# Optimization experiments

Measured on AMD Instinct MI355X. Metric: run time of the kernel, lower is better.

Reference implementation:

```python
import jax, jax.numpy as jnp
import numpy as np

B, T, H, L, V = 256, 1024, 256, 128, 13  # V = FDIM_JOINT_VOCAB_DECODING


def setup_inputs() -> dict:
    key = jax.random.key(0)
    ks = jax.random.split(key, 16)
    s = lambda *sh: 1.0 / np.sqrt(sh[-1])
    inp = {
        "seq_input": jax.random.normal(ks[0], (B, T, V), jnp.float32),
        "latent_vec": jax.random.normal(ks[1], (B, L), jnp.float32),
        "labels": jax.random.randint(ks[2], (B, T), 0, V, jnp.int32),
        "lengths": jax.random.randint(ks[3], (B,), 1, T, jnp.int32),
        # latent_vec_linear: L -> H
        "W_lat": jax.random.normal(ks[4], (H, L), jnp.float32) * s(H, L),
        "b_lat": jnp.zeros((H,), jnp.float32),
        # LSTMCell (PyTorch gate order i,f,g,o)
        "W_ih": jax.random.normal(ks[5], (4 * H, V), jnp.float32) * s(4 * H, V),
        "W_hh": jax.random.normal(ks[6], (4 * H, H), jnp.float32) * s(4 * H, H),
        "b_ih": jnp.zeros((4 * H,), jnp.float32),
        "b_hh": jnp.zeros((4 * H,), jnp.float32),
        # W_nonlinear: H+L -> H
        "W_nl": jax.random.normal(ks[7], (H, H + L), jnp.float32) * s(H, H + L),
        "b_nl": jnp.zeros((H,), jnp.float32),
        # W: H -> V
        "W_out": jax.random.normal(ks[8], (V, H), jnp.float32) * s(V, H),
        "b_out": jnp.zeros((V,), jnp.float32),
    }
    return inp


def _forward(seq_input, latent_vec, labels, lengths,
             W_lat, b_lat, W_ih, W_hh, b_ih, b_hh, W_nl, b_nl, W_out, b_out):
    h0 = jax.nn.relu(latent_vec @ W_lat.T + b_lat)          # [B,H]
    c0 = jnp.zeros_like(h0)

    def step(carry, x_t):
        h, c = carry
        gates = x_t @ W_ih.T + b_ih + h @ W_hh.T + b_hh     # [B,4H]
        i, f, g, o = jnp.split(gates, 4, axis=-1)
        c = jax.nn.sigmoid(f) * c + jax.nn.sigmoid(i) * jnp.tanh(g)
        h = jax.nn.sigmoid(o) * jnp.tanh(c)
        return (h, c), h

    xs = jnp.swapaxes(seq_input, 0, 1)                      # [T,B,V]
    _, hs = jax.lax.scan(step, (h0, c0), xs)                # [T,B,H]
    hs = jnp.swapaxes(hs, 0, 1)                             # [B,T,H]

    lat = jnp.broadcast_to(latent_vec[:, None, :], (B, T, L))
    feats = jnp.concatenate([hs, lat], axis=-1)             # [B,T,H+L]
    logits = jax.nn.relu(feats @ W_nl.T + b_nl) @ W_out.T + b_out  # [B,T,V]

    logp = jax.nn.log_softmax(logits, axis=-1)
    nll = -jnp.take_along_axis(logp, labels[..., None], axis=-1)[..., 0]  # [B,T]
    mask = (jnp.arange(T)[None, :] < lengths[:, None]).astype(nll.dtype)
    batch_loss = jnp.sum(nll * mask, axis=1)                # [B]
    return batch_loss


def reference(seq_input, latent_vec, labels, lengths,
              W_lat, b_lat, W_ih, W_hh, b_ih, b_hh, W_nl, b_nl, W_out, b_out):
    return _forward(seq_input, latent_vec, labels, lengths,
                    W_lat, b_lat, W_ih, W_hh, b_ih, b_hh, W_nl, b_nl, W_out, b_out)
```

## Files before the change

kernel.cpp:

```cpp
#include <hip/hip_runtime.h>
#include <hip/hip_fp16.h>

#define NB 256
#define NT 1024
#define NH 256
#define NL 128
#define NV 13

typedef _Float16 h2t __attribute__((ext_vector_type(2)));
typedef _Float16 f16x8 __attribute__((ext_vector_type(8)));
typedef float f32x4 __attribute__((ext_vector_type(4)));

#define WS_WHH   0x0u
#define WS_WIH   0x80000u
#define WS_BIAS  0x88000u
#define WS_H0F   0x89000u
#define WS_LATF  0xA9000u
#define WS_WNL   0xB9000u
#define WS_WOUT  0xE9000u
#define WS_HS    0x100000u

__device__ __forceinline__ unsigned pk2(float a, float b){
  union { h2t h; unsigned u; } u;
  u.h.x = (_Float16)a; u.h.y = (_Float16)b;
  return u.u;
}

__device__ __forceinline__ float fdot2u(unsigned a, unsigned b, float c){
#if __has_builtin(__builtin_amdgcn_fdot2)
  union { unsigned u; h2t h; } ua, ub;
  ua.u = a; ub.u = b;
  return __builtin_amdgcn_fdot2(ua.h, ub.h, c, false);
#else
  union { unsigned u; h2t h; } ua, ub;
  ua.u = a; ub.u = b;
  return c + (float)ua.h.x*(float)ub.h.x + (float)ua.h.y*(float)ub.h.y;
#endif
}

__device__ __forceinline__ float sigm(float x){ return __builtin_amdgcn_rcpf(1.f + __expf(-x)); }
__device__ __forceinline__ float tanh_(float x){ return 2.f*__builtin_amdgcn_rcpf(1.f + __expf(-2.f*x)) - 1.f; }

__global__ void k_prep(const float* __restrict__ Wih, const float* __restrict__ Whh,
                       const float* __restrict__ bih, const float* __restrict__ bhh,
                       const float* __restrict__ Wnl, const float* __restrict__ Wout,
                       unsigned char* __restrict__ ws){
  unsigned* whh = (unsigned*)(ws + WS_WHH);
  unsigned* wih = (unsigned*)(ws + WS_WIH);
  float* bias   = (float*)(ws + WS_BIAS);
  unsigned* wnl = (unsigned*)(ws + WS_WNL);
  unsigned* wout= (unsigned*)(ws + WS_WOUT);
  int blk = blockIdx.x, tid = threadIdx.x;
  if (blk < 1024){
    int r = blk;
    if (tid < 128) whh[r*128+tid] = pk2(Whh[r*256+2*tid], Whh[r*256+2*tid+1]);
    if (tid < 8){
      int k0 = 2*tid, k1 = 2*tid+1;
      float a = (k0 < NV)? Wih[r*NV+k0] : 0.f;
      float b = (k1 < NV)? Wih[r*NV+k1] : 0.f;
      wih[r*8+tid] = pk2(a,b);
    }
    if (tid == 0) bias[r] = bih[r] + bhh[r];
  } else if (blk < 1280){
    int n = blk - 1024;
    for (int i = tid; i < 192; i += 128)
      wnl[n*192+i] = pk2(Wnl[n*384+2*i], Wnl[n*384+2*i+1]);
  } else {
    for (int i = tid; i < 2048; i += 128){
      int v = i >> 7; int p = (i & 127)*2;
      float a = (v < NV)? Wout[v*256+p]   : 0.f;
      float b = (v < NV)? Wout[v*256+p+1] : 0.f;
      wout[i] = pk2(a,b);
    }
  }
}

__global__ void k_init(const float* __restrict__ lat, const float* __restrict__ Wlat,
                       const float* __restrict__ blat, unsigned char* __restrict__ ws,
                       float* __restrict__ out){
  __shared__ float sl[NL];
  __shared__ float h0[NH];
  int b = blockIdx.x, j = threadIdx.x;
  if (j < NL) sl[j] = lat[b*NL+j];
  __syncthreads();
  float a = blat[j];
  for (int k = 0; k < NL; ++k) a += Wlat[j*NL+k]*sl[k];
  h0[j] = a > 0.f ? a : 0.f;
  __syncthreads();
  unsigned* h0f  = (unsigned*)(ws + WS_H0F);
  unsigned* latf = (unsigned*)(ws + WS_LATF);
  if (j < 128) h0f[b*128+j] = pk2(h0[2*j], h0[2*j+1]);
  if (j < 64)  latf[b*64+j] = pk2(sl[2*j], sl[2*j+1]);
  if (j == 0)  out[b] = 0.f;
}

__global__ __launch_bounds__(512, 2)
void k_lstm(const float* __restrict__ seq, unsigned char* __restrict__ ws){
  __shared__ __align__(16) unsigned lw[1024*36];
  __shared__ __align__(16) unsigned h2[128];
  __shared__ float gts[1024];
  __shared__ unsigned xb[2][8];
  int b = blockIdx.x, j = threadIdx.x;
  int r0 = j, r1 = j + 512;
  const uint4* whh4 = (const uint4*)(ws + WS_WHH);
  const uint4* wih4 = (const uint4*)(ws + WS_WIH);
  const float* bias = (const float*)(ws + WS_BIAS);
  const unsigned* h0f = (const unsigned*)(ws + WS_H0F);
  __half* hs = (__half*)(ws + WS_HS);

  uint4 w0v[24], w1v[24];
#pragma unroll
  for (int i = 0; i < 24; ++i){ w0v[i] = whh4[r0*32+i]; w1v[i] = whh4[r1*32+i]; }
  uint4* lw4 = (uint4*)lw;
#pragma unroll
  for (int i = 0; i < 8; ++i){ lw4[r0*9+i] = whh4[r0*32+24+i]; lw4[r1*9+i] = whh4[r1*32+24+i]; }
  uint4 wi0a = wih4[r0*2], wi0b = wih4[r0*2+1];
  uint4 wi1a = wih4[r1*2], wi1b = wih4[r1*2+1];
  float bb0 = bias[r0], bb1 = bias[r1];
  if (j < 128) h2[j] = h0f[b*128+j];
  if (j >= 256 && j < 264){
    int i2 = j - 256; int k0 = 2*i2;
    const float* xp = seq + (size_t)b*NT*NV;
    float xa = (k0   < NV)? xp[k0]   : 0.f;
    float xc = (k0+1 < NV)? xp[k0+1] : 0.f;
    xb[0][i2] = pk2(xa, xc);
  }
  float c = 0.f;
  __syncthreads();
  const uint4* h2v = (const uint4*)h2;

#pragma unroll 1
  for (int t = 0; t < NT; ++t){
    float a0 = bb0, a1 = bb1;
    {
      const unsigned* xc = xb[t & 1];
      a0 = fdot2u(wi0a.x, xc[0], a0); a0 = fdot2u(wi0a.y, xc[1], a0);
      a0 = fdot2u(wi0a.z, xc[2], a0); a0 = fdot2u(wi0a.w, xc[3], a0);
      a0 = fdot2u(wi0b.x, xc[4], a0); a0 = fdot2u(wi0b.y, xc[5], a0);
      a0 = fdot2u(wi0b.z, xc[6], a0);
      a1 = fdot2u(wi1a.x, xc[0], a1); a1 = fdot2u(wi1a.y, xc[1], a1);
      a1 = fdot2u(wi1a.z, xc[2], a1); a1 = fdot2u(wi1a.w, xc[3], a1);
      a1 = fdot2u(wi1b.x, xc[4], a1); a1 = fdot2u(wi1b.y, xc[5], a1);
      a1 = fdot2u(wi1b.z, xc[6], a1);
    }
#pragma unroll
    for (int q = 0; q < 24; ++q){
      uint4 hq = h2v[q];
      a0 = fdot2u(w0v[q].x, hq.x, a0); a0 = fdot2u(w0v[q].y, hq.y, a0);
      a0 = fdot2u(w0v[q].z, hq.z, a0); a0 = fdot2u(w0v[q].w, hq.w, a0);
      a1 = fdot2u(w1v[q].x, hq.x, a1); a1 = fdot2u(w1v[q].y, hq.y, a1);
      a1 = fdot2u(w1v[q].z, hq.z, a1); a1 = fdot2u(w1v[q].w, hq.w, a1);
    }
#pragma unroll
    for (int q = 0; q < 8; ++q){
      uint4 hq = h2v[24+q];
      uint4 wa = lw4[r0*9+q];
      uint4 wb = lw4[r1*9+q];
      a0 = fdot2u(wa.x, hq.x, a0); a0 = fdot2u(wa.y, hq.y, a0);
      a0 = fdot2u(wa.z, hq.z, a0); a0 = fdot2u(wa.w, hq.w, a0);
      a1 = fdot2u(wb.x, hq.x, a1); a1 = fdot2u(wb.y, hq.y, a1);
      a1 = fdot2u(wb.z, hq.z, a1); a1 = fdot2u(wb.w, hq.w, a1);
    }
    gts[r0] = a0; gts[r1] = a1;

    unsigned xpk = 0;
    bool doX = (j >= 256 && j < 264) && (t+1 < NT);
    if (doX){
      int i2 = j - 256; int k0 = 2*i2;
      const float* xp = seq + ((size_t)b*NT + (t+1))*NV;
      float xa = (k0   < NV)? xp[k0]   : 0.f;
      float xc2= (k0+1 < NV)? xp[k0+1] : 0.f;
      xpk = pk2(xa, xc2);
    }
    __syncthreads();
    if (j < 256){
      float gi = gts[j], gf = gts[j+256], gg = gts[j+512], go = gts[j+768];
      c = sigm(gf)*c + sigm(gi)*tanh_(gg);
      float h = sigm(go)*tanh_(c);
      __half hh = __float2half(h);
      ((__half*)h2)[j] = hh;
      hs[((size_t)b*NT + t)*NH + j] = hh;
    }
    if (doX) xb[(t+1) & 1][j-256] = xpk;
    __syncthreads();
  }
}

struct __align__(16) SMp {
  union {
    struct { __half As[128][72]; __half Bs[256][72]; } s;
    __half Zs[128][264];
  } u;
  unsigned wout[16][128];
  float bnl[256];
  float bout[16];
  float logit[128][16];
  float red[128];
};

__global__ __launch_bounds__(512, 2)
void k_proj(const unsigned char* __restrict__ ws,
            const int* __restrict__ labels, const int* __restrict__ lengths,
            const float* __restrict__ bnl, const float* __restrict__ bout,
            float* __restrict__ out){
  __shared__ SMp sm;
  int tid = threadIdx.x;
  int mt = blockIdx.x;
  int m0 = mt*128;
  int b  = m0 >> 10;
  int t0 = m0 & 1023;
  const __half* hs      = (const __half*)(ws + WS_HS);
  const unsigned* latf  = (const unsigned*)(ws + WS_LATF);
  const unsigned* wnl   = (const unsigned*)(ws + WS_WNL);
  const unsigned* woutg = (const unsigned*)(ws + WS_WOUT);

  for (int i = tid; i < 2048; i += 512) ((unsigned*)sm.wout)[i] = woutg[i];
  if (tid < 256) sm.bnl[tid] = bnl[tid];
  if (tid < 16)  sm.bout[tid] = (tid < NV)? bout[tid] : 0.f;

  int wave = tid >> 6, lane = tid & 63;
  int wm = wave >> 2, wn = wave & 3;
  int l15 = lane & 15, l4 = lane >> 4;

  f32x4 acc[4][4];
  f32x4 zz = {0.f,0.f,0.f,0.f};
#pragma unroll
  for (int a = 0; a < 4; ++a)
#pragma unroll
    for (int q = 0; q < 4; ++q) acc[a][q] = zz;

#pragma unroll 1
  for (int kt = 0; kt < 6; ++kt){
#pragma unroll
    for (int it = 0; it < 2; ++it){
      int idx = it*512 + tid;
      int r = idx >> 3, ck = idx & 7;
      int k = kt*64 + ck*8;
      uint4 val;
      if (k < 256) val = *(const uint4*)&hs[((size_t)(m0+r))*NH + k];
      else         val = *(const uint4*)&latf[b*64 + (k-256)/2];
      *(uint4*)&sm.u.s.As[r][ck*8] = val;
    }
#pragma unroll
    for (int it = 0; it < 4; ++it){
      int idx = it*512 + tid;
      int n = idx >> 3, ck = idx & 7;
      int k = kt*64 + ck*8;
      uint4 val = *(const uint4*)&wnl[n*192 + k/2];
      *(uint4*)&sm.u.s.Bs[n][ck*8] = val;
    }
    __syncthreads();
#pragma unroll
    for (int kk = 0; kk < 2; ++kk){
      f16x8 af[4], bf[4];
#pragma unroll
      for (int mf = 0; mf < 4; ++mf) af[mf] = *(const f16x8*)&sm.u.s.As[wm*64+mf*16+l15][kk*32+l4*8];
#pragma unroll
      for (int nf = 0; nf < 4; ++nf) bf[nf] = *(const f16x8*)&sm.u.s.Bs[wn*64+nf*16+l15][kk*32+l4*8];
#pragma unroll
      for (int mf = 0; mf < 4; ++mf)
#pragma unroll
        for (int nf = 0; nf < 4; ++nf)
          acc[mf][nf] = __builtin_amdgcn_mfma_f32_16x16x32_f16(af[mf], bf[nf], acc[mf][nf], 0, 0, 0);
    }
    __syncthreads();
  }

#pragma unroll
  for (int mf = 0; mf < 4; ++mf)
#pragma unroll
    for (int nf = 0; nf < 4; ++nf)
#pragma unroll
      for (int e = 0; e < 4; ++e){
        int row = wm*64 + mf*16 + l4*4 + e;
        int col = wn*64 + nf*16 + l15;
        float v = acc[mf][nf][e] + sm.bnl[col];
        v = v > 0.f ? v : 0.f;
        sm.u.Zs[row][col] = __float2half(v);
      }
  __syncthreads();

  int r = tid >> 2, q = tid & 3;
  float la0 = sm.bout[q], la1 = sm.bout[q+4], la2 = sm.bout[q+8], la3 = sm.bout[q+12];
#pragma unroll
  for (int c8 = 0; c8 < 32; ++c8){
    uint4 zv = *(const uint4*)&sm.u.Zs[r][c8*8];
    uint4 w0 = *(const uint4*)&sm.wout[q][c8*4];
    uint4 w1 = *(const uint4*)&sm.wout[q+4][c8*4];
    uint4 w2 = *(const uint4*)&sm.wout[q+8][c8*4];
    uint4 w3 = *(const uint4*)&sm.wout[q+12][c8*4];
    la0 = fdot2u(w0.x, zv.x, la0); la0 = fdot2u(w0.y, zv.y, la0);
    la0 = fdot2u(w0.z, zv.z, la0); la0 = fdot2u(w0.w, zv.w, la0);
    la1 = fdot2u(w1.x, zv.x, la1); la1 = fdot2u(w1.y, zv.y, la1);
    la1 = fdot2u(w1.z, zv.z, la1); la1 = fdot2u(w1.w, zv.w, la1);
    la2 = fdot2u(w2.x, zv.x, la2); la2 = fdot2u(w2.y, zv.y, la2);
    la2 = fdot2u(w2.z, zv.z, la2); la2 = fdot2u(w2.w, zv.w, la2);
    la3 = fdot2u(w3.x, zv.x, la3); la3 = fdot2u(w3.y, zv.y, la3);
    la3 = fdot2u(w3.z, zv.z, la3); la3 = fdot2u(w3.w, zv.w, la3);
  }
  sm.logit[r][q] = la0; sm.logit[r][q+4] = la1; sm.logit[r][q+8] = la2; sm.logit[r][q+12] = la3;
  __syncthreads();

  if (tid < 128){
    int t = t0 + tid;
    float mx = -1e30f;
#pragma unroll
    for (int v = 0; v < NV; ++v) mx = fmaxf(mx, sm.logit[tid][v]);
    float s = 0.f;
#pragma unroll
    for (int v = 0; v < NV; ++v) s += __expf(sm.logit[tid][v] - mx);
    float lse = mx + __logf(s);
    int lab = labels[b*NT + t];
    float nll = lse - sm.logit[tid][lab];
    sm.red[tid] = (t < lengths[b])? nll : 0.f;
  }
  __syncthreads();
  if (tid < 64){
    float v = sm.red[tid] + sm.red[tid+64];
#pragma unroll
    for (int off = 32; off > 0; off >>= 1) v += __shfl_down(v, off);
    if (tid == 0) atomicAdd(out + b, v);
  }
}

extern "C" void kernel_launch(void* const* d_in, const int* in_sizes, int n_in,
                              void* d_out, int out_size, void* d_ws, size_t ws_size,
                              hipStream_t stream){
  const float* seq   = (const float*)d_in[0];
  const float* lat   = (const float*)d_in[1];
  const int* labels  = (const int*)d_in[2];
  const int* lengths = (const int*)d_in[3];
  const float* Wlat  = (const float*)d_in[4];
  const float* blat  = (const float*)d_in[5];
  const float* Wih   = (const float*)d_in[6];
  const float* Whh   = (const float*)d_in[7];
  const float* bih   = (const float*)d_in[8];
  const float* bhh   = (const float*)d_in[9];
  const float* Wnl   = (const float*)d_in[10];
  const float* bnl   = (const float*)d_in[11];
  const float* Wout  = (const float*)d_in[12];
  const float* bout  = (const float*)d_in[13];
  float* out = (float*)d_out;
  unsigned char* ws = (unsigned char*)d_ws;

  hipLaunchKernelGGL(k_prep, dim3(1281), dim3(128), 0, stream, Wih, Whh, bih, bhh, Wnl, Wout, ws);
  hipLaunchKernelGGL(k_init, dim3(256), dim3(256), 0, stream, lat, Wlat, blat, ws, out);
  hipLaunchKernelGGL(k_lstm, dim3(256), dim3(512), 0, stream, seq, ws);
  hipLaunchKernelGGL(k_proj, dim3(2048), dim3(512), 0, stream, ws, labels, lengths, bnl, bout, out);
}
```

Measured before the change: 2.340 ms.

## Keep i/g gates in registers, split accumulators, and transpose LDS weight layout

Threads 0-255 already compute gates i and g in registers, so only threads 256-511 now publish f and o through a smaller shared array. This cuts LDS traffic before the barrier. Each dot product is split into two independent accumulator chains to shorten the fdot2 dependency latency. The LDS-resident weight tail is transposed to a [q][thread] layout to avoid bank conflicts. Empty asm statements pin the weights in VGPRs, and waves_per_eu is fixed at 2, which risks higher register pressure.

```diff
diff --git a/kernel.cpp b/kernel.cpp
--- a/kernel.cpp
+++ b/kernel.cpp
@@ -27,15 +27,9 @@
 }
 
 __device__ __forceinline__ float fdot2u(unsigned a, unsigned b, float c){
-#if __has_builtin(__builtin_amdgcn_fdot2)
   union { unsigned u; h2t h; } ua, ub;
   ua.u = a; ub.u = b;
   return __builtin_amdgcn_fdot2(ua.h, ub.h, c, false);
-#else
-  union { unsigned u; h2t h; } ua, ub;
-  ua.u = a; ub.u = b;
-  return c + (float)ua.h.x*(float)ub.h.x + (float)ua.h.y*(float)ub.h.y;
-#endif
 }
 
 __device__ __forceinline__ float sigm(float x){ return __builtin_amdgcn_rcpf(1.f + __expf(-x)); }
@@ -94,12 +88,13 @@
   if (j == 0)  out[b] = 0.f;
 }
 
-__global__ __launch_bounds__(512, 2)
+__global__ __launch_bounds__(512) __attribute__((amdgpu_waves_per_eu(2, 2)))
 void k_lstm(const float* __restrict__ seq, unsigned char* __restrict__ ws){
-  __shared__ __align__(16) unsigned lw[1024*36];
+  __shared__ __align__(16) uint4 lwA[8][512];
+  __shared__ __align__(16) uint4 lwB[8][512];
   __shared__ __align__(16) unsigned h2[128];
-  __shared__ float gts[1024];
-  __shared__ unsigned xb[2][8];
+  __shared__ __align__(8)  float gts2[256][2];
+  __shared__ __align__(16) unsigned xb[2][8];
   int b = blockIdx.x, j = threadIdx.x;
   int r0 = j, r1 = j + 512;
   const uint4* whh4 = (const uint4*)(ws + WS_WHH);
@@ -108,14 +103,13 @@
   const unsigned* h0f = (const unsigned*)(ws + WS_H0F);
   __half* hs = (__half*)(ws + WS_HS);
 
-  uint4 w0v[24], w1v[24];
-#pragma unroll
-  for (int i = 0; i < 24; ++i){ w0v[i] = whh4[r0*32+i]; w1v[i] = whh4[r1*32+i]; }
-  uint4* lw4 = (uint4*)lw;
-#pragma unroll
-  for (int i = 0; i < 8; ++i){ lw4[r0*9+i] = whh4[r0*32+24+i]; lw4[r1*9+i] = whh4[r1*32+24+i]; }
-  uint4 wi0a = wih4[r0*2], wi0b = wih4[r0*2+1];
-  uint4 wi1a = wih4[r1*2], wi1b = wih4[r1*2+1];
+  uint4 wa_[24], wb_[24];
+#pragma unroll
+  for (int i = 0; i < 24; ++i){ wa_[i] = whh4[r0*32+i]; wb_[i] = whh4[r1*32+i]; }
+#pragma unroll
+  for (int q = 0; q < 8; ++q){ lwA[q][j] = whh4[r0*32+24+q]; lwB[q][j] = whh4[r1*32+24+q]; }
+  uint4 wx0a = wih4[r0*2], wx0b = wih4[r0*2+1];
+  uint4 wx1a = wih4[r1*2], wx1b = wih4[r1*2+1];
   float bb0 = bias[r0], bb1 = bias[r1];
   if (j < 128) h2[j] = h0f[b*128+j];
   if (j >= 256 && j < 264){
@@ -126,42 +120,55 @@
     xb[0][i2] = pk2(xa, xc);
   }
   float c = 0.f;
+#pragma unroll
+  for (int i = 0; i < 24; ++i){
+    asm volatile("" : "+v"(wa_[i].x), "+v"(wa_[i].y), "+v"(wa_[i].z), "+v"(wa_[i].w));
+    asm volatile("" : "+v"(wb_[i].x), "+v"(wb_[i].y), "+v"(wb_[i].z), "+v"(wb_[i].w));
+  }
+  asm volatile("" : "+v"(wx0a.x), "+v"(wx0a.y), "+v"(wx0a.z), "+v"(wx0a.w));
+  asm volatile("" : "+v"(wx0b.x), "+v"(wx0b.y), "+v"(wx0b.z), "+v"(wx0b.w));
+  asm volatile("" : "+v"(wx1a.x), "+v"(wx1a.y), "+v"(wx1a.z), "+v"(wx1a.w));
+  asm volatile("" : "+v"(wx1b.x), "+v"(wx1b.y), "+v"(wx1b.z), "+v"(wx1b.w));
   __syncthreads();
   const uint4* h2v = (const uint4*)h2;
 
 #pragma unroll 1
   for (int t = 0; t < NT; ++t){
-    float a0 = bb0, a1 = bb1;
+    float p00 = bb0, p01 = 0.f;
+    float p10 = bb1, p11 = 0.f;
     {
-      const unsigned* xc = xb[t & 1];
-      a0 = fdot2u(wi0a.x, xc[0], a0); a0 = fdot2u(wi0a.y, xc[1], a0);
-      a0 = fdot2u(wi0a.z, xc[2], a0); a0 = fdot2u(wi0a.w, xc[3], a0);
-      a0 = fdot2u(wi0b.x, xc[4], a0); a0 = fdot2u(wi0b.y, xc[5], a0);
-      a0 = fdot2u(wi0b.z, xc[6], a0);
-      a1 = fdot2u(wi1a.x, xc[0], a1); a1 = fdot2u(wi1a.y, xc[1], a1);
-      a1 = fdot2u(wi1a.z, xc[2], a1); a1 = fdot2u(wi1a.w, xc[3], a1);
-      a1 = fdot2u(wi1b.x, xc[4], a1); a1 = fdot2u(wi1b.y, xc[5], a1);
-      a1 = fdot2u(wi1b.z, xc[6], a1);
+      const uint4* xc4 = (const uint4*)xb[t & 1];
+      uint4 x0 = xc4[0], x1 = xc4[1];
+      p00 = fdot2u(wx0a.x, x0.x, p00); p01 = fdot2u(wx0a.y, x0.y, p01);
+      p00 = fdot2u(wx0a.z, x0.z, p00); p01 = fdot2u(wx0a.w, x0.w, p01);
+      p00 = fdot2u(wx0b.x, x1.x, p00); p01 = fdot2u(wx0b.y, x1.y, p01);
+      p00 = fdot2u(wx0b.z, x1.z, p00);
+      p10 = fdot2u(wx1a.x, x0.x, p10); p11 = fdot2u(wx1a.y, x0.y, p11);
+      p10 = fdot2u(wx1a.z, x0.z, p10); p11 = fdot2u(wx1a.w, x0.w, p11);
+      p10 = fdot2u(wx1b.x, x1.x, p10); p11 = fdot2u(wx1b.y, x1.y, p11);
+      p10 = fdot2u(wx1b.z, x1.z, p10);
     }
 #pragma unroll
     for (int q = 0; q < 24; ++q){
       uint4 hq = h2v[q];
-      a0 = fdot2u(w0v[q].x, hq.x, a0); a0 = fdot2u(w0v[q].y, hq.y, a0);
-      a0 = fdot2u(w0v[q].z, hq.z, a0); a0 = fdot2u(w0v[q].w, hq.w, a0);
-      a1 = fdot2u(w1v[q].x, hq.x, a1); a1 = fdot2u(w1v[q].y, hq.y, a1);
-      a1 = fdot2u(w1v[q].z, hq.z, a1); a1 = fdot2u(w1v[q].w, hq.w, a1);
+      p00 = fdot2u(wa_[q].x, hq.x, p00); p01 = fdot2u(wa_[q].y, hq.y, p01);
+      p00 = fdot2u(wa_[q].z, hq.z, p00); p01 = fdot2u(wa_[q].w, hq.w, p01);
+      p10 = fdot2u(wb_[q].x, hq.x, p10); p11 = fdot2u(wb_[q].y, hq.y, p11);
+      p10 = fdot2u(wb_[q].z, hq.z, p10); p11 = fdot2u(wb_[q].w, hq.w, p11);
     }
 #pragma unroll
     for (int q = 0; q < 8; ++q){
       uint4 hq = h2v[24+q];
-      uint4 wa = lw4[r0*9+q];
-      uint4 wb = lw4[r1*9+q];
-      a0 = fdot2u(wa.x, hq.x, a0); a0 = fdot2u(wa.y, hq.y, a0);
-      a0 = fdot2u(wa.z, hq.z, a0); a0 = fdot2u(wa.w, hq.w, a0);
-      a1 = fdot2u(wb.x, hq.x, a1); a1 = fdot2u(wb.y, hq.y, a1);
-      a1 = fdot2u(wb.z, hq.z, a1); a1 = fdot2u(wb.w, hq.w, a1);
-    }
-    gts[r0] = a0; gts[r1] = a1;
+      uint4 wa = lwA[q][j];
+      uint4 wb = lwB[q][j];
+      p00 = fdot2u(wa.x, hq.x, p00); p01 = fdot2u(wa.y, hq.y, p01);
+      p00 = fdot2u(wa.z, hq.z, p00); p01 = fdot2u(wa.w, hq.w, p01);
+      p10 = fdot2u(wb.x, hq.x, p10); p11 = fdot2u(wb.y, hq.y, p11);
+      p10 = fdot2u(wb.z, hq.z, p10); p11 = fdot2u(wb.w, hq.w, p11);
+    }
+    float a0 = p00 + p01;
+    float a1 = p10 + p11;
+    if (j >= 256){ *(float2*)gts2[j-256] = make_float2(a0, a1); }
 
     unsigned xpk = 0;
     bool doX = (j >= 256 && j < 264) && (t+1 < NT);
@@ -174,8 +181,9 @@
     }
     __syncthreads();
     if (j < 256){
-      float gi = gts[j], gf = gts[j+256], gg = gts[j+512], go = gts[j+768];
-      c = sigm(gf)*c + sigm(gi)*tanh_(gg);
+      float2 fo = *(const float2*)gts2[j];
+      float gf = fo.x, go = fo.y;
+      c = sigm(gf)*c + sigm(a0)*tanh_(a1);
       float h = sigm(go)*tanh_(c);
       __half hh = __float2half(h);
       ((__half*)h2)[j] = hh;
```

Result: slower. 2.459 ms (+5.1%).
